# Kernel optimization log

Measured on AMD Instinct MI355X. Metric: run time of the kernel, lower is better.

## Reference

```python
import math
import jax, jax.numpy as jnp
import numpy as np

B_, L_, D_, N_, R_ = 4, 1024, 1024, 16, 64  # batch, seq, n_embd(=dim_inner), d_state, dt_rank


def setup_inputs() -> dict:
    key = jax.random.key(0)
    ks = jax.random.split(key, 6)
    s = lambda k, shp: jax.random.normal(k, shp, jnp.float32) * 0.02
    return {
        "x": jax.random.normal(ks[0], (B_, L_, D_), jnp.float32),
        "ln1_w": jnp.ones((D_,), jnp.float32),
        "ln2_w": jnp.ones((D_,), jnp.float32),
        "W_dbc": s(ks[1], (R_ + 2 * N_, D_)),   # x -> [delta_lowrank, B, C]
        "W_dt": s(ks[2], (D_, R_)),              # dt_rank -> dim_inner
        "b_dt": jnp.zeros((D_,), jnp.float32),
        "A_log": jnp.log(jnp.broadcast_to(jnp.arange(1, N_ + 1, dtype=jnp.float32), (D_, N_))),
        "Dp": jnp.ones((D_,), jnp.float32),      # skip-connection D parameter
        "W_fc": s(ks[3], (4 * D_, D_)),
        "W_proj": s(ks[4], (D_, 4 * D_)),
    }


def _layernorm(x, w):
    mu = jnp.mean(x, -1, keepdims=True)
    xc = x - mu
    var = jnp.mean(xc * xc, -1, keepdims=True)
    return xc * jax.lax.rsqrt(var + 1e-5) * w


def _new_gelu(x):
    c = math.sqrt(2.0 / math.pi)
    return 0.5 * x * (1.0 + jnp.tanh(c * (x + 0.044715 * x * x * x)))


def _ssm(x, W_dbc, W_dt, b_dt, A_log, Dp):
    # x: (b, l, d) with d == dim_inner == n_embd
    dbc = jnp.einsum("bld,ed->ble", x, W_dbc)                # (b,l,R+2N)
    delta, Bm, Cm = jnp.split(dbc, [R_, R_ + N_], axis=-1)
    delta = jax.nn.softplus(jnp.einsum("blr,dr->bld", delta, W_dt) + b_dt)  # (b,l,d)
    A = -jnp.exp(A_log)                                       # (d,n)
    dA = jnp.exp(delta[..., None] * A)                        # (b,l,d,n) discretized A
    dBx = (delta * x)[..., None] * Bm[:, :, None, :]          # (b,l,d,n) discretized B*x

    # h_t = dA_t * h_{t-1} + dBx_t  -> parallel first-order linear scan
    def combine(e1, e2):
        a1, b1 = e1
        a2, b2 = e2
        return a2 * a1, a2 * b1 + b2

    _, hs = jax.lax.associative_scan(combine, (dA, dBx), axis=1)
    y = jnp.einsum("bldn,bln->bld", hs, Cm)
    return y + x * Dp


def reference(x, ln1_w, ln2_w, W_dbc, W_dt, b_dt, A_log, Dp, W_fc, W_proj):
    h = jax.nn.softplus(_layernorm(x, ln1_w))
    h = h + _ssm(h, W_dbc, W_dt, b_dt, A_log, Dp)
    m = _layernorm(h, ln2_w)
    m = _new_gelu(jnp.einsum("bld,fd->blf", m, W_fc))
    m = jnp.einsum("blf,df->bld", m, W_proj)
    return h + m
```

## Files before the change

### kernel.cpp

```cpp
#include <hip/hip_runtime.h>
#include <cstdint>
#include <cstddef>

typedef unsigned short u16;
typedef unsigned int u32;
typedef __attribute__((ext_vector_type(8))) short short8;
typedef __attribute__((ext_vector_type(4))) float floatx4;
typedef __attribute__((ext_vector_type(4))) u16 u16x4;

#define DEV static __device__ __forceinline__

DEV u16 f2b(float f){ u32 u = __float_as_uint(f); u32 r = u + 0x7fffu + ((u>>16)&1u); return (u16)(r>>16); }
DEV float softplusf(float z){ return fmaxf(z,0.f) + log1pf(__expf(-fabsf(z))); }
DEV float fast_tanhf(float u){ float e = __expf(2.f*u); return 1.f - 2.f/(e+1.f); }
DEV float geluf(float x){ float u = 0.7978845608028654f*(x + 0.044715f*x*x*x); return 0.5f*x*(1.f+fast_tanhf(u)); }

DEV void async_copy16(const void* gp, void* lp){
  __builtin_amdgcn_global_load_lds((const __attribute__((address_space(1))) u32*)gp,
                                   (__attribute__((address_space(3))) u32*)lp, 16, 0, 0);
}

__global__ __launch_bounds__(256)
void prep_weights(const float* __restrict__ Wdbc, const float* __restrict__ Wdt,
                  const float* __restrict__ Wfc, const float* __restrict__ Wproj,
                  u16* __restrict__ dbc_b, u16* __restrict__ dt_b,
                  u16* __restrict__ fc_b, u16* __restrict__ pj_b)
{
  int i = blockIdx.x*256 + threadIdx.x;
  const float* src; u16* dst; int j;
  if (i < 32768){
    int e = i*4, r = e >> 10;
    if (r >= 96){ u16x4 z = {0,0,0,0}; *(u16x4*)(dbc_b + e) = z; return; }
    src = Wdbc; dst = dbc_b; j = i;
  } else if (i < 49152){ src = Wdt;   dst = dt_b; j = i - 32768; }
  else if (i < 1097728){ src = Wfc;   dst = fc_b; j = i - 49152; }
  else                 { src = Wproj; dst = pj_b; j = i - 1097728; }
  float4 v = ((const float4*)src)[j];
  u16x4 o = { f2b(v.x), f2b(v.y), f2b(v.z), f2b(v.w) };
  *(u16x4*)(dst + j*4) = o;
}

__global__ void dbc_post(const float* __restrict__ p, u16* __restrict__ delta_in,
                         float* __restrict__ BCf){
  int e = blockIdx.x*256 + threadIdx.x;
  int t = e >> 7, c = e & 127;
  float s = 0.f;
  #pragma unroll
  for (int z=0;z<8;z++) s += p[(size_t)z*524288 + e];
  if (c < 64)      delta_in[t*64 + c] = f2b(s);
  else if (c < 96) BCf[t*32 + (c-64)] = s;
}

__global__ void proj_reduce(const float* __restrict__ p, const float* __restrict__ h1f,
                            float* __restrict__ out){
  int i = blockIdx.x*256 + threadIdx.x;
  float4 a = ((const float4*)p)[i];
  float4 b = ((const float4*)(p + (size_t)4194304))[i];
  float4 r = ((const float4*)h1f)[i];
  float4 o = make_float4(a.x+b.x+r.x, a.y+b.y+r.y, a.z+b.z+r.z, a.w+b.w+r.w);
  ((float4*)out)[i] = o;
}

__global__ __launch_bounds__(256)
void ln1_kernel(const float* __restrict__ x, const float* __restrict__ w,
                float* __restrict__ h0f, u16* __restrict__ h0b)
{
  int row = blockIdx.x, tid = threadIdx.x;
  const float4* xr = (const float4*)(x + (size_t)row*1024);
  float4 v = xr[tid];
  float s1 = v.x+v.y+v.z+v.w;
  float s2 = v.x*v.x+v.y*v.y+v.z*v.z+v.w*v.w;
  #pragma unroll
  for (int m=1;m<64;m<<=1){ s1 += __shfl_xor(s1,m); s2 += __shfl_xor(s2,m); }
  __shared__ float red[8];
  int wv = tid>>6;
  if ((tid&63)==0){ red[wv]=s1; red[4+wv]=s2; }
  __syncthreads();
  s1 = red[0]+red[1]+red[2]+red[3];
  s2 = red[4]+red[5]+red[6]+red[7];
  float mu  = s1*(1.f/1024.f);
  float var = s2*(1.f/1024.f) - mu*mu;
  float rstd = rsqrtf(var + 1e-5f);
  float4 wv4 = ((const float4*)w)[tid];
  float o0 = softplusf((v.x-mu)*rstd*wv4.x);
  float o1 = softplusf((v.y-mu)*rstd*wv4.y);
  float o2 = softplusf((v.z-mu)*rstd*wv4.z);
  float o3 = softplusf((v.w-mu)*rstd*wv4.w);
  ((float4*)(h0f + (size_t)row*1024))[tid] = make_float4(o0,o1,o2,o3);
  u16x4 ob = { f2b(o0), f2b(o1), f2b(o2), f2b(o3) };
  *(u16x4*)(h0b + (size_t)row*1024 + tid*4) = ob;
}

__global__ __launch_bounds__(256)
void ln2_kernel(const float* __restrict__ x, const float* __restrict__ w,
                u16* __restrict__ outb)
{
  int row = blockIdx.x, tid = threadIdx.x;
  const float4* xr = (const float4*)(x + (size_t)row*1024);
  float4 v = xr[tid];
  float s1 = v.x+v.y+v.z+v.w;
  float s2 = v.x*v.x+v.y*v.y+v.z*v.z+v.w*v.w;
  #pragma unroll
  for (int m=1;m<64;m<<=1){ s1 += __shfl_xor(s1,m); s2 += __shfl_xor(s2,m); }
  __shared__ float red[8];
  int wv = tid>>6;
  if ((tid&63)==0){ red[wv]=s1; red[4+wv]=s2; }
  __syncthreads();
  s1 = red[0]+red[1]+red[2]+red[3];
  s2 = red[4]+red[5]+red[6]+red[7];
  float mu  = s1*(1.f/1024.f);
  float var = s2*(1.f/1024.f) - mu*mu;
  float rstd = rsqrtf(var + 1e-5f);
  float4 wv4 = ((const float4*)w)[tid];
  u16x4 ob = { f2b((v.x-mu)*rstd*wv4.x), f2b((v.y-mu)*rstd*wv4.y),
               f2b((v.z-mu)*rstd*wv4.z), f2b((v.w-mu)*rstd*wv4.w) };
  *(u16x4*)(outb + (size_t)row*1024 + tid*4) = ob;
}

template<int EPI, int SWZ>
__global__ __launch_bounds__(256)
void gemm_bt(const u16* __restrict__ A, int lda,
             const u16* __restrict__ B, int ldb, int K,
             float* __restrict__ outF, u16* __restrict__ outB, int ldo,
             const float* __restrict__ bias, size_t zstr)
{
  __shared__ u16 sA[128*32];
  __shared__ u16 sB[128*32];
  const int tid = threadIdx.x;
  int m_blk, n_blk, zb;
  if (SWZ == 0){ n_blk = blockIdx.x; m_blk = blockIdx.y; zb = blockIdx.z; }
  else if (SWZ == 1){
    int b = blockIdx.x, xcd = b & 7, local = b >> 3;
    m_blk = (xcd>>2)*16 + (local & 15);
    n_blk = (xcd&3)*8 + (local >> 4);
    zb = 0;
  } else {
    int b = blockIdx.x, xcd = b & 7, local = b >> 3;
    m_blk = (xcd>>1)*8 + (local & 7);
    n_blk = local >> 3;
    zb = xcd & 1;
  }
  const int m0 = m_blk*128, n0 = n_blk*128;
  const int kstart = zb * K;
  const int wave = tid>>6, lane = tid&63;
  const int wm = (wave>>1)*64, wn = (wave&1)*64;
  const int lr = lane&15, quad = lane>>4;

  floatx4 acc[4][4];
  #pragma unroll
  for (int i=0;i<4;i++)
    #pragma unroll
    for (int j=0;j<4;j++){ floatx4 z = {0.f,0.f,0.f,0.f}; acc[i][j]=z; }

  const int r0 = tid>>2;
  const int kc8 = (((tid&3) ^ ((tid>>3)&3)))*8;
  const int sswz = ((lr>>1)&3);
  for (int k0=kstart; k0<kstart+K; k0+=32){
    __syncthreads();
    async_copy16(A + (size_t)(m0+r0)*lda    + k0+kc8, &sA[(size_t)tid*8]);
    async_copy16(A + (size_t)(m0+64+r0)*lda + k0+kc8, &sA[(size_t)(tid+256)*8]);
    async_copy16(B + (size_t)(n0+r0)*ldb    + k0+kc8, &sB[(size_t)tid*8]);
    async_copy16(B + (size_t)(n0+64+r0)*ldb + k0+kc8, &sB[(size_t)(tid+256)*8]);
    __syncthreads();
    short8 af[4], bf[4];
    #pragma unroll
    for (int i=0;i<4;i++){
      af[i] = *(const short8*)&sA[(wm+i*16+lr)*32 + (quad^sswz)*8];
      bf[i] = *(const short8*)&sB[(wn+i*16+lr)*32 + (quad^sswz)*8];
    }
    #pragma unroll
    for (int i=0;i<4;i++)
      #pragma unroll
      for (int j=0;j<4;j++)
        acc[i][j] = __builtin_amdgcn_mfma_f32_16x16x32_bf16(af[i], bf[j], acc[i][j], 0,0,0);
  }
  #pragma unroll
  for (int i=0;i<4;i++){
    #pragma unroll
    for (int j=0;j<4;j++){
      #pragma unroll
      for (int r=0;r<4;r++){
        int gr = m0 + wm + i*16 + quad*4 + r;
        int gc = n0 + wn + j*16 + lr;
        float v = acc[i][j][r];
        size_t o = (size_t)gr*ldo + gc;
        if (EPI==1)      outF[o] = softplusf(v + bias[gc]);
        else if (EPI==2) outB[o] = f2b(geluf(v));
        else             outF[zstr*zb + o] = v;
      }
    }
  }
}

__global__ __launch_bounds__(256)
void scan_p1(const float* __restrict__ delta, const float* __restrict__ h0f,
             const float* __restrict__ BCf, const float* __restrict__ A_log,
             float* __restrict__ Pbuf, float* __restrict__ Sbuf)
{
  int blk = blockIdx.x;
  int d = (blk & 3)*256 + threadIdx.x;
  int c = (blk >> 2) & 31;
  int b = blk >> 7;
  float a2[16], h[16], P[16];
  #pragma unroll
  for (int n=0;n<16;n++){ a2[n] = -__expf(A_log[d*16+n]) * 1.44269504f; h[n]=0.f; P[n]=1.f; }
  int t0 = c*32;
  const float* dptr = delta + ((size_t)(b*1024 + t0))*1024 + d;
  const float* xptr = h0f   + ((size_t)(b*1024 + t0))*1024 + d;
  const float* bc   = BCf   + ((size_t)(b*1024 + t0))*32;
  #pragma unroll 4
  for (int t=0;t<32;t++){
    float dlt = dptr[t*1024];
    float xv  = xptr[t*1024];
    float dx = dlt*xv;
    #pragma unroll
    for (int n=0;n<16;n++){
      float dA = exp2f(dlt*a2[n]);
      h[n] = dA*h[n] + dx*bc[t*32+n];
      P[n] *= dA;
    }
  }
  size_t base = ((size_t)((b*32 + c)*16))*1024 + d;
  #pragma unroll
  for (int n=0;n<16;n++){ Pbuf[base + (size_t)n*1024] = P[n]; Sbuf[base + (size_t)n*1024] = h[n]; }
}

__global__ __launch_bounds__(256)
void scan_p2(const float* __restrict__ Pbuf, const float* __restrict__ Sbuf,
             float* __restrict__ Hbuf)
{
  int blk = blockIdx.x;
  int d = (blk & 3)*256 + threadIdx.x;
  int n = (blk >> 2) & 15;
  int b = blk >> 6;
  float H = 0.f;
  for (int c=0;c<32;c++){
    size_t idx = ((size_t)((b*32 + c)*16 + n))*1024 + d;
    float P = Pbuf[idx], S = Sbuf[idx];
    Hbuf[idx] = H;
    H = P*H + S;
  }
}

__global__ __launch_bounds__(256)
void scan_p3(const float* __restrict__ delta, const float* __restrict__ h0f,
             const float* __restrict__ BCf, const float* __restrict__ A_log,
             const float* __restrict__ Hbuf, const float* __restrict__ Dp,
             float* __restrict__ h1f)
{
  int blk = blockIdx.x;
  int d = (blk & 3)*256 + threadIdx.x;
  int c = (blk >> 2) & 31;
  int b = blk >> 7;
  float a2[16], h[16];
  size_t hb = ((size_t)((b*32 + c)*16))*1024 + d;
  #pragma unroll
  for (int n=0;n<16;n++){
    a2[n] = -__expf(A_log[d*16+n]) * 1.44269504f;
    h[n] = Hbuf[hb + (size_t)n*1024];
  }
  float dpv = 1.f + Dp[d];
  int t0 = c*32;
  const float* dptr = delta + ((size_t)(b*1024 + t0))*1024 + d;
  const float* xptr = h0f   + ((size_t)(b*1024 + t0))*1024 + d;
  const float* bc   = BCf   + ((size_t)(b*1024 + t0))*32;
  float* optr = h1f + ((size_t)(b*1024 + t0))*1024 + d;
  #pragma unroll 4
  for (int t=0;t<32;t++){
    float dlt = dptr[t*1024];
    float xv  = xptr[t*1024];
    float dx = dlt*xv;
    float y = 0.f;
    #pragma unroll
    for (int n=0;n<16;n++){
      float dA = exp2f(dlt*a2[n]);
      h[n] = dA*h[n] + dx*bc[t*32+n];
      y += h[n]*bc[t*32+16+n];
    }
    optr[t*1024] = xv*dpv + y;
  }
}

extern "C" void kernel_launch(void* const* d_in, const int* in_sizes, int n_in,
                              void* d_out, int out_size, void* d_ws, size_t ws_size,
                              hipStream_t stream)
{
  const float* x    = (const float*)d_in[0];
  const float* ln1w = (const float*)d_in[1];
  const float* ln2w = (const float*)d_in[2];
  const float* Wdbc = (const float*)d_in[3];
  const float* Wdt  = (const float*)d_in[4];
  const float* bdt  = (const float*)d_in[5];
  const float* Alog = (const float*)d_in[6];
  const float* Dp   = (const float*)d_in[7];
  const float* Wfc  = (const float*)d_in[8];
  const float* Wproj= (const float*)d_in[9];
  float* out = (float*)d_out;

  char* ws = (char*)d_ws;
  size_t off = 0;
  auto carve = [&](size_t bytes)->char*{ char* p = ws + off; off += (bytes + 255) & ~(size_t)255; return p; };
  const size_t T = 4096;
  float* h0f   = (float*)carve(T*1024*4);
  float* h1f   = (float*)carve(T*1024*4);
  float* dlt   = (float*)carve(T*1024*4);
  float* Pbuf  = (float*)carve((size_t)4*32*16*1024*4);
  float* Sbuf  = (float*)carve((size_t)4*32*16*1024*4);
  float* Hbuf  = (float*)carve((size_t)4*32*16*1024*4);
  float* pad_  = (float*)carve((size_t)4*32*16*1024*4);
  float* BCf   = (float*)carve(T*32*4);
  u16*   h0b   = (u16*)  carve(T*1024*2);
  u16*   m0b   = (u16*)  carve(T*1024*2);
  u16*   g_b   = (u16*)  carve(T*4096*2);
  u16*   din_b = (u16*)  carve(T*64*2);
  u16*   Wdbc_b= (u16*)  carve((size_t)128*1024*2);
  u16*   Wdt_b = (u16*)  carve((size_t)1024*64*2);
  u16*   Wfc_b = (u16*)  carve((size_t)4096*1024*2);
  u16*   Wpj_b = (u16*)  carve((size_t)1024*4096*2);
  float* dbc_p  = Hbuf;
  float* proj_p = Pbuf;
  (void)pad_; (void)ws_size; (void)in_sizes; (void)n_in; (void)out_size;

  prep_weights<<<8384, 256, 0, stream>>>(Wdbc, Wdt, Wfc, Wproj,
                                         Wdbc_b, Wdt_b, Wfc_b, Wpj_b);

  ln1_kernel<<<4096, 256, 0, stream>>>(x, ln1w, h0f, h0b);

  gemm_bt<4,0><<<dim3(1,32,8), 256, 0, stream>>>(h0b, 1024, Wdbc_b, 1024, 128,
                                                 dbc_p, nullptr, 128, nullptr, (size_t)T*128);
  dbc_post<<<2048, 256, 0, stream>>>(dbc_p, din_b, BCf);

  gemm_bt<1,0><<<dim3(8,32), 256, 0, stream>>>(din_b, 64, Wdt_b, 64, 64,
                                               dlt, nullptr, 1024, bdt, 0);

  scan_p1<<<512, 256, 0, stream>>>(dlt, h0f, BCf, Alog, Pbuf, Sbuf);
  scan_p2<<<256, 256, 0, stream>>>(Pbuf, Sbuf, Hbuf);
  scan_p3<<<512, 256, 0, stream>>>(dlt, h0f, BCf, Alog, Hbuf, Dp, h1f);

  ln2_kernel<<<4096, 256, 0, stream>>>(h1f, ln2w, m0b);

  gemm_bt<2,1><<<1024, 256, 0, stream>>>(m0b, 1024, Wfc_b, 1024, 1024,
                                         nullptr, g_b, 4096, nullptr, 0);

  gemm_bt<4,2><<<512, 256, 0, stream>>>(g_b, 4096, Wpj_b, 4096, 2048,
                                        proj_p, nullptr, 1024, nullptr, (size_t)T*1024);
  proj_reduce<<<4096, 256, 0, stream>>>(proj_p, h1f, out);
}
```

Measured before the change: 356.1 us.

## Use 256x256-tile 512-thread GEMM with XCD swizzle for MLP matmuls

Adds a new GEMM kernel with 256x256 output tiles, 8 waves, a double-buffered LDS pipeline split into four phases with async global-to-LDS loads, swizzled LDS layout and MFMA priority hints. Uses it for both MLP projections, with block-to-XCD mapping meant to improve L2 reuse. The down-projection switches from split-K 2 to split-K 4, so the reduce kernel now sums four partials, and the partial buffer is moved to the larger delta buffer. The aim is higher arithmetic intensity and fewer launches' worth of tile reloads, at the cost of more registers (two blocks per CU) and extra reduction traffic.

```diff
diff --git a/kernel.cpp b/kernel.cpp
--- a/kernel.cpp
+++ b/kernel.cpp
@@ -55,9 +55,12 @@
                             float* __restrict__ out){
   int i = blockIdx.x*256 + threadIdx.x;
   float4 a = ((const float4*)p)[i];
-  float4 b = ((const float4*)(p + (size_t)4194304))[i];
+  float4 b = ((const float4*)(p + (size_t) 4194304))[i];
+  float4 c = ((const float4*)(p + (size_t) 8388608))[i];
+  float4 d = ((const float4*)(p + (size_t)12582912))[i];
   float4 r = ((const float4*)h1f)[i];
-  float4 o = make_float4(a.x+b.x+r.x, a.y+b.y+r.y, a.z+b.z+r.z, a.w+b.w+r.w);
+  float4 o = make_float4(a.x+b.x+c.x+d.x+r.x, a.y+b.y+c.y+d.y+r.y,
+                         a.z+b.z+c.z+d.z+r.z, a.w+b.w+c.w+d.w+r.w);
   ((float4*)out)[i] = o;
 }
 
@@ -187,6 +190,128 @@
         if (EPI==1)      outF[o] = softplusf(v + bias[gc]);
         else if (EPI==2) outB[o] = f2b(geluf(v));
         else             outF[zstr*zb + o] = v;
+      }
+    }
+  }
+}
+
+template<int EPI, int SWZ>
+__global__ __launch_bounds__(512, 2)
+void gemm256(const u16* __restrict__ A, int lda,
+             const u16* __restrict__ B, int ldb, int K,
+             float* __restrict__ outF, u16* __restrict__ outB, int ldo,
+             size_t zstr)
+{
+  __shared__ u16 sA[2][4][4096];
+  __shared__ u16 sB[2][4][4096];
+  const int tid = threadIdx.x;
+  int m_blk, n_blk, zb;
+  if (SWZ == 3){
+    int b = blockIdx.x, xcd = b & 7, local = b >> 3;
+    m_blk = (xcd>>2)*8 + (local & 7);
+    n_blk = (xcd&3)*4 + (local >> 3);
+    zb = 0;
+  } else {
+    int b = blockIdx.x, xcd = b & 7, local = b >> 3;
+    zb    = xcd >> 1;
+    m_blk = (xcd&1)*8 + (local & 7);
+    n_blk = local >> 3;
+  }
+  const int m0 = m_blk*256, n0 = n_blk*256;
+  const int kstart = zb*K;
+  const int wave = tid>>6, lane = tid&63;
+  const int mq = wave>>2, nq = wave&3;
+  const int lr = lane&15, quad = lane>>4;
+  const int sswz = (lr>>1)&3;
+
+  const int srow = tid>>2;
+  const int scol = ((tid&3) ^ ((tid>>3)&3))*8;
+  const u16* pa = A + (size_t)(m0 + srow)*lda + scol;
+  const u16* pb = B + (size_t)(n0 + srow)*ldb + scol;
+  u16* la = (u16*)sA + tid*8;
+  u16* lb = (u16*)sB + tid*8;
+  const size_t ah128 = (size_t)128*lda;
+  const size_t bh128 = (size_t)128*ldb;
+
+  const int a_rd = (mq*64 + lr)*32 + (quad^sswz)*8;
+  const int b_rd = ((nq&1)*64 + lr)*32 + (quad^sswz)*8;
+  const int bun  = nq>>1;
+
+  floatx4 acc[2][4][4];
+  #pragma unroll
+  for (int h=0;h<2;h++)
+    #pragma unroll
+    for (int i=0;i<4;i++)
+      #pragma unroll
+      for (int j=0;j<4;j++){ floatx4 z={0.f,0.f,0.f,0.f}; acc[h][i][j]=z; }
+
+#define STG_A(NB,KS,H,KT) async_copy16(pa + (size_t)(H)*ah128 + (size_t)((KT) + (KS)*32), \
+                                       la + (NB)*16384 + ((KS)*2+(H))*4096)
+#define STG_B(NB,KS,H,KT) async_copy16(pb + (size_t)(H)*bh128 + (size_t)((KT) + (KS)*32), \
+                                       lb + (NB)*16384 + ((KS)*2+(H))*4096)
+
+#define PHASE(CUR, KA, AH, VM, ...)                                           \
+  {                                                                           \
+    asm volatile("s_waitcnt vmcnt(" VM ")" ::: "memory");                     \
+    asm volatile("s_barrier" ::: "memory");                                   \
+    __VA_ARGS__;                                                              \
+    const u16* ca = (const u16*)sA + (CUR)*16384 + ((KA)*2+(AH))*4096;        \
+    const u16* cb = (const u16*)sB + (CUR)*16384 + ((KA)*2+bun)*4096;         \
+    short8 af[4], bf[4];                                                      \
+    _Pragma("unroll")                                                         \
+    for (int i_=0;i_<4;i_++){                                                 \
+      af[i_] = *(const short8*)(ca + a_rd + i_*512);                          \
+      bf[i_] = *(const short8*)(cb + b_rd + i_*512);                          \
+    }                                                                         \
+    __builtin_amdgcn_s_setprio(1);                                            \
+    _Pragma("unroll")                                                         \
+    for (int i_=0;i_<4;i_++)                                                  \
+      _Pragma("unroll")                                                       \
+      for (int j_=0;j_<4;j_++)                                                \
+        acc[AH][i_][j_] = __builtin_amdgcn_mfma_f32_16x16x32_bf16(            \
+            af[i_], bf[j_], acc[AH][i_][j_], 0,0,0);                          \
+    __builtin_amdgcn_s_setprio(0);                                            \
+  }
+
+  STG_A(0,0,0,kstart); STG_B(0,0,0,kstart);
+  STG_B(0,0,1,kstart); STG_A(0,0,1,kstart);
+  STG_B(0,1,0,kstart); STG_B(0,1,1,kstart);
+  STG_A(0,1,0,kstart); STG_A(0,1,1,kstart);
+
+  const int NT = K >> 6;
+  int cur = 0;
+  int ktn = kstart + 64;
+  for (int t=0; t<NT-1; ++t, ktn += 64, cur ^= 1){
+    const int nb = cur^1;
+    PHASE(cur, 0,0, "5", STG_A(nb,0,0,ktn); STG_B(nb,0,0,ktn));
+    PHASE(cur, 0,1, "6", STG_B(nb,0,1,ktn); STG_A(nb,0,1,ktn));
+    PHASE(cur, 1,0, "5", STG_B(nb,1,0,ktn); STG_B(nb,1,1,ktn));
+    PHASE(cur, 1,1, "6", STG_A(nb,1,0,ktn); STG_A(nb,1,1,ktn));
+  }
+  PHASE(cur, 0,0, "5", );
+  PHASE(cur, 0,1, "4", );
+  PHASE(cur, 1,0, "1", );
+  PHASE(cur, 1,1, "0", );
+
+#undef PHASE
+#undef STG_A
+#undef STG_B
+
+  #pragma unroll
+  for (int h=0;h<2;h++){
+    #pragma unroll
+    for (int i=0;i<4;i++){
+      #pragma unroll
+      for (int j=0;j<4;j++){
+        #pragma unroll
+        for (int r=0;r<4;r++){
+          int gr = m0 + h*128 + mq*64 + i*16 + quad*4 + r;
+          int gc = n0 + nq*64 + j*16 + lr;
+          float v = acc[h][i][j][r];
+          size_t o = (size_t)gr*ldo + gc;
+          if (EPI==2) outB[o] = f2b(geluf(v));
+          else        outF[zstr*zb + o] = v;
+        }
       }
     }
   }
@@ -318,7 +443,7 @@
   u16*   Wfc_b = (u16*)  carve((size_t)4096*1024*2);
   u16*   Wpj_b = (u16*)  carve((size_t)1024*4096*2);
   float* dbc_p  = Hbuf;
-  float* proj_p = Pbuf;
+  float* proj_p = dlt;
   (void)pad_; (void)ws_size; (void)in_sizes; (void)n_in; (void)out_size;
 
   prep_weights<<<8384, 256, 0, stream>>>(Wdbc, Wdt, Wfc, Wproj,
@@ -339,10 +464,10 @@
 
   ln2_kernel<<<4096, 256, 0, stream>>>(h1f, ln2w, m0b);
 
-  gemm_bt<2,1><<<1024, 256, 0, stream>>>(m0b, 1024, Wfc_b, 1024, 1024,
-                                         nullptr, g_b, 4096, nullptr, 0);
-
-  gemm_bt<4,2><<<512, 256, 0, stream>>>(g_b, 4096, Wpj_b, 4096, 2048,
-                                        proj_p, nullptr, 1024, nullptr, (size_t)T*1024);
+  gemm256<2,3><<<256, 512, 0, stream>>>(m0b, 1024, Wfc_b, 1024, 1024,
+                                        nullptr, g_b, 4096, 0);
+
+  gemm256<4,4><<<256, 512, 0, stream>>>(g_b, 4096, Wpj_b, 4096, 1024,
+                                        proj_p, nullptr, 1024, (size_t)T*1024);
   proj_reduce<<<4096, 256, 0, stream>>>(proj_p, h1f, out);
 }
```

Result: no change. 356.0 us (-0.0%).
